# Kernel optimization log

Hardware: AMD Instinct MI355X
Metric: run time of the kernel (lower is better)

Reference implementation:

```python
import jax, jax.numpy as jnp
import numpy as np

N_NODES = 50000
N_EDGES = 800000
N_GRAPHS = 1024
NODE_IN = 128
HID = 300
DEPTH = 5
READOUT = 1024


def setup_inputs() -> dict:
    key = jax.random.key(0)
    ks = jax.random.split(key, 12)
    x = jax.random.normal(ks[0], (N_NODES, NODE_IN), dtype=jnp.float32)
    edge_index = jax.random.randint(ks[1], (2, N_EDGES), 0, N_NODES, dtype=jnp.int32)
    batch = jnp.sort(jax.random.randint(ks[2], (N_NODES,), 0, N_GRAPHS, dtype=jnp.int32))
    s_in = 1.0 / np.sqrt(NODE_IN)
    s_h = 1.0 / np.sqrt(HID)
    W_proj = jax.random.normal(ks[3], (NODE_IN, HID), dtype=jnp.float32) * s_in
    b_proj = jnp.zeros((HID,), dtype=jnp.float32)
    W1 = jax.random.normal(ks[4], (DEPTH, HID, HID), dtype=jnp.float32) * s_h
    b1 = jnp.zeros((DEPTH, HID), dtype=jnp.float32)
    W2 = jax.random.normal(ks[5], (DEPTH, HID, HID), dtype=jnp.float32) * s_h
    b2 = jnp.zeros((DEPTH, HID), dtype=jnp.float32)
    W_sp = jax.random.normal(ks[6], (HID, READOUT), dtype=jnp.float32) * s_h
    b_sp = jnp.zeros((READOUT,), dtype=jnp.float32)
    prelu_a = jnp.full((1,), 0.25, dtype=jnp.float32)  # nn.PReLU default
    return {"x": x, "edge_index": edge_index, "batch": batch,
            "W_proj": W_proj, "b_proj": b_proj, "W1": W1, "b1": b1,
            "W2": W2, "b2": b2, "W_sp": W_sp, "b_sp": b_sp, "prelu_a": prelu_a}


def reference(x, edge_index, batch, W_proj, b_proj, W1, b1, W2, b2, W_sp, b_sp, prelu_a):
    # project_node_feats: Linear + ReLU
    h = jax.nn.relu(x @ W_proj + b_proj)  # [N, HID]
    src = edge_index[0]
    dst = edge_index[1]
    for i in range(DEPTH):
        # GINConv (eps=0): out = nn(x + sum_{j in N(i)} x_j)
        agg = h + jax.ops.segment_sum(h[src], dst, num_segments=N_NODES)
        h = jax.nn.relu(agg @ W1[i] + b1[i]) @ W2[i] + b2[i]
        if i < DEPTH - 1:
            h = jax.nn.relu(h)
        # dropout is identity in eval mode
    # global_add_pool over graph ids
    pooled = jax.ops.segment_sum(h, batch, num_segments=N_GRAPHS)  # [G, HID]
    z = pooled @ W_sp + b_sp  # [G, READOUT]
    # PReLU with single shared parameter
    readout = jnp.where(z >= 0, z, prelu_a[0] * z)
    return readout
```

## Files before the change

kernel.cpp:

```cpp
#include <hip/hip_runtime.h>
#include <cstdint>

#define N_NODES 50000
#define N_EDGES 800000
#define N_GRAPHS 1024
#define NODE_IN 128
#define HID 300
#define DEPTH 5
#define READOUT 1024
#define PSTR 320

typedef float f32x4 __attribute__((ext_vector_type(4)));
typedef short bf16x8 __attribute__((ext_vector_type(8)));
typedef unsigned short us8 __attribute__((ext_vector_type(8)));

__device__ inline unsigned short f2bf(float v) {
    unsigned u = __float_as_uint(v);
    unsigned r = u + 0x7FFFu + ((u >> 16) & 1u);
    return (unsigned short)(r >> 16);
}
__device__ inline float bf2f(unsigned short h) {
    return __uint_as_float((unsigned)h << 16);
}
__device__ inline float bflo(unsigned u) { return __uint_as_float(u << 16); }
__device__ inline float bfhi(unsigned u) { return __uint_as_float(u & 0xFFFF0000u); }
__device__ inline unsigned packbf(float a, float b) {
    return (unsigned)f2bf(a) | ((unsigned)f2bf(b) << 16);
}

__global__ void hist2(const int* __restrict__ dst, int* __restrict__ cnt,
                      const int* __restrict__ batch, int* __restrict__ gcnt) {
    int i = blockIdx.x * blockDim.x + threadIdx.x;
    if (i < N_EDGES) atomicAdd(&cnt[dst[i]], 1);
    else if (i < N_EDGES + N_NODES) atomicAdd(&gcnt[batch[i - N_EDGES]], 1);
}

__global__ __launch_bounds__(256)
void scan_block2(const int* __restrict__ cnt, int* __restrict__ offs, int* __restrict__ bsum,
                 const int* __restrict__ gcnt, int* __restrict__ goffs, int* __restrict__ gsum,
                 int nbn) {
    __shared__ int buf[256];
    int b = blockIdx.x;
    const int* in; int* out; int* bs; int n; int bi;
    if (b < nbn) { in = cnt; out = offs; bs = bsum; n = N_NODES; bi = b; }
    else { in = gcnt; out = goffs; bs = gsum; n = N_GRAPHS; bi = b - nbn; }
    int i = bi * 256 + (int)threadIdx.x;
    int v = (i < n) ? in[i] : 0;
    buf[threadIdx.x] = v;
    __syncthreads();
    for (int off = 1; off < 256; off <<= 1) {
        int t = ((int)threadIdx.x >= off) ? buf[threadIdx.x - off] : 0;
        __syncthreads();
        buf[threadIdx.x] += t;
        __syncthreads();
    }
    if (i < n) out[i] = buf[threadIdx.x] - v;
    if (threadIdx.x == 255) bs[bi] = buf[255];
}

__global__ __launch_bounds__(256)
void scan_base2(const int* __restrict__ bsum, int* __restrict__ bbase, int nbn, int* __restrict__ tot_n,
                const int* __restrict__ gsum, int* __restrict__ gbase, int nbg, int* __restrict__ tot_g) {
    __shared__ int buf[256];
    const int* bs; int* bb; int nb; int* tot;
    if (blockIdx.x == 0) { bs = bsum; bb = bbase; nb = nbn; tot = tot_n; }
    else { bs = gsum; bb = gbase; nb = nbg; tot = tot_g; }
    int v = ((int)threadIdx.x < nb) ? bs[threadIdx.x] : 0;
    buf[threadIdx.x] = v;
    __syncthreads();
    for (int off = 1; off < 256; off <<= 1) {
        int t = ((int)threadIdx.x >= off) ? buf[threadIdx.x - off] : 0;
        __syncthreads();
        buf[threadIdx.x] += t;
        __syncthreads();
    }
    if ((int)threadIdx.x < nb) bb[threadIdx.x] = buf[threadIdx.x] - v;
    if (threadIdx.x == 255) *tot = buf[255];
}

__global__ void scan_add2(int* __restrict__ offs, const int* __restrict__ bbase,
                          int* __restrict__ cursor,
                          int* __restrict__ goffs, const int* __restrict__ gbase, int nbn) {
    int b = blockIdx.x;
    if (b < nbn) {
        int i = b * 256 + (int)threadIdx.x;
        if (i < N_NODES) {
            int o = offs[i] + bbase[b];
            offs[i] = o;
            cursor[i] = o;
        }
    } else {
        int bi = b - nbn;
        int i = bi * 256 + (int)threadIdx.x;
        if (i < N_GRAPHS) goffs[i] += gbase[bi];
    }
}

__global__ void scatter_kernel(const int* __restrict__ src, const int* __restrict__ dst,
                               int* __restrict__ cursor, int* __restrict__ csr, int n) {
    int i = blockIdx.x * blockDim.x + threadIdx.x;
    if (i < n) {
        int p = atomicAdd(&cursor[dst[i]], 1);
        csr[p] = src[i];
    }
}

__global__ __launch_bounds__(256)
void aggregate_bf16(const unsigned short* __restrict__ h, const int* __restrict__ offs,
                    const int* __restrict__ csr, unsigned short* __restrict__ out) {
    int wave = (int)((blockIdx.x * blockDim.x + threadIdx.x) >> 6);
    int lane = threadIdx.x & 63;
    if (wave >= N_NODES) return;
    float a0, a1, a2, a3, a4, a5;
    {
        const unsigned* r = (const unsigned*)(h + (size_t)wave * PSTR);
        uint2 u = *(const uint2*)&r[2 * lane];
        unsigned t = (lane < 32) ? r[128 + lane] : 0u;
        a0 = bflo(u.x); a1 = bfhi(u.x);
        a2 = bflo(u.y); a3 = bfhi(u.y);
        a4 = bflo(t);   a5 = bfhi(t);
    }
    int s = offs[wave], e = offs[wave + 1];
    int k = s;
    for (; k + 3 < e; k += 4) {
        const unsigned* r0 = (const unsigned*)(h + (size_t)csr[k] * PSTR);
        const unsigned* r1 = (const unsigned*)(h + (size_t)csr[k + 1] * PSTR);
        const unsigned* r2 = (const unsigned*)(h + (size_t)csr[k + 2] * PSTR);
        const unsigned* r3 = (const unsigned*)(h + (size_t)csr[k + 3] * PSTR);
        uint2 x0 = *(const uint2*)&r0[2 * lane];
        uint2 x1 = *(const uint2*)&r1[2 * lane];
        uint2 x2 = *(const uint2*)&r2[2 * lane];
        uint2 x3 = *(const uint2*)&r3[2 * lane];
        unsigned t0 = 0, t1 = 0, t2 = 0, t3 = 0;
        if (lane < 32) {
            t0 = r0[128 + lane]; t1 = r1[128 + lane];
            t2 = r2[128 + lane]; t3 = r3[128 + lane];
        }
        a0 += bflo(x0.x) + bflo(x1.x) + bflo(x2.x) + bflo(x3.x);
        a1 += bfhi(x0.x) + bfhi(x1.x) + bfhi(x2.x) + bfhi(x3.x);
        a2 += bflo(x0.y) + bflo(x1.y) + bflo(x2.y) + bflo(x3.y);
        a3 += bfhi(x0.y) + bfhi(x1.y) + bfhi(x2.y) + bfhi(x3.y);
        a4 += bflo(t0) + bflo(t1) + bflo(t2) + bflo(t3);
        a5 += bfhi(t0) + bfhi(t1) + bfhi(t2) + bfhi(t3);
    }
    for (; k < e; ++k) {
        const unsigned* r = (const unsigned*)(h + (size_t)csr[k] * PSTR);
        uint2 u = *(const uint2*)&r[2 * lane];
        unsigned t = (lane < 32) ? r[128 + lane] : 0u;
        a0 += bflo(u.x); a1 += bfhi(u.x);
        a2 += bflo(u.y); a3 += bfhi(u.y);
        a4 += bflo(t);   a5 += bfhi(t);
    }
    unsigned* o = (unsigned*)(out + (size_t)wave * PSTR);
    uint2 w; w.x = packbf(a0, a1); w.y = packbf(a2, a3);
    *(uint2*)&o[2 * lane] = w;
    if (lane < 32) o[128 + lane] = (lane < 22) ? packbf(a4, a5) : 0u;
}

__global__ __launch_bounds__(256)
void split_all(const float* __restrict__ W1, const float* __restrict__ W2,
               const float* __restrict__ Wsp, const float* __restrict__ Wproj,
               unsigned short* __restrict__ w1S, unsigned short* __restrict__ w2S,
               unsigned short* __restrict__ spH, unsigned short* __restrict__ spL,
               unsigned short* __restrict__ pjH, unsigned short* __restrict__ pjL) {
    __shared__ float tile[32][33];
    const int STK_SZ = 320 * 640;
    int z = blockIdx.z;
    const float* W;
    int K, N;
    if (z < 10) {
        if (blockIdx.x >= 10) return;
        int l = z % 5;
        W = (z < 5 ? W1 : W2) + (size_t)l * HID * HID;
        K = HID; N = HID;
    } else if (z == 10) {
        W = Wsp; K = HID; N = READOUT;
    } else {
        if (blockIdx.x >= 10 || blockIdx.y >= 4) return;
        W = Wproj; K = NODE_IN; N = HID;
    }
    int n0 = blockIdx.x * 32, k0 = blockIdx.y * 32;
    int tx = threadIdx.x & 31, ty = threadIdx.x >> 5;
#pragma unroll
    for (int r = 0; r < 4; ++r) {
        int k = k0 + ty + r * 8, n = n0 + tx;
        tile[ty + r * 8][tx] = (k < K && n < N) ? W[(size_t)k * N + n] : 0.f;
    }
    __syncthreads();
#pragma unroll
    for (int r = 0; r < 4; ++r) {
        int n = n0 + ty + r * 8, k = k0 + tx;
        float v = tile[tx][ty + r * 8];
        unsigned short hb = f2bf(v);
        unsigned short lb = f2bf(v - bf2f(hb));
        if (z < 10) {
            unsigned short* S = (z < 5 ? w1S : w2S) + (size_t)(z % 5) * STK_SZ;
            S[(size_t)n * 640 + k] = hb;
            S[(size_t)n * 640 + 320 + k] = lb;
        } else if (z == 10) {
            spH[(size_t)n * 320 + k] = hb;
            spL[(size_t)n * 320 + k] = lb;
        } else {
            pjH[(size_t)n * 128 + k] = hb;
            pjL[(size_t)n * 128 + k] = lb;
        }
    }
}

#define BSWZ(r, c) ((c) ^ (((r) >> 1) & 3))

__global__ __launch_bounds__(512, 1)
void gin_mlp_bk64(const unsigned short* __restrict__ Ap, int M,
                  const unsigned short* __restrict__ B1, const float* __restrict__ b1,
                  const unsigned short* __restrict__ B2, const float* __restrict__ b2,
                  unsigned short* __restrict__ Op, int act2) {
    __shared__ __align__(16) unsigned short At[128 * 320];
    __shared__ __align__(16) unsigned short Bs[2 * 320 * 64];

    const int tid = threadIdx.x;
    const int bm = blockIdx.x * 128;
    const int wid = tid >> 6, lane = tid & 63;
    const int wm = wid >> 2, wn = wid & 3;
    const int lr = lane & 15, lk = lane >> 4;

    float b1v[5], b2v[5];
#pragma unroll
    for (int n = 0; n < 5; ++n) {
        int col = wn * 80 + n * 16 + lr;
        b1v[n] = (col < HID) ? b1[col] : 0.f;
        b2v[n] = (col < HID) ? b2[col] : 0.f;
    }

    size_t bofs[10]; int bldso[10];
#pragma unroll
    for (int i = 0; i < 10; ++i) {
        int q = i * 512 + tid;
        int half = q >= 2560;
        int q2 = q - half * 2560;
        int r = q2 >> 3, c = q2 & 7;
        bofs[i] = (size_t)r * 640 + half * 320 + c * 8;
        bldso[i] = half * 20480 + r * 64 + ((c ^ (r & 7)) * 8);
    }

    us8 vB[10];
    auto LOADB = [&](const unsigned short* B, int t) {
        int k0 = t * 64;
#pragma unroll
        for (int i = 0; i < 10; ++i)
            vB[i] = *(const us8*)&B[bofs[i] + k0];
    };

    LOADB(B1, 0);

#pragma unroll
    for (int i = 0; i < 10; ++i) {
        int g = i * 512 + tid;
        int row = g / 40, c = g - row * 40;
        int grow = bm + row; if (grow >= M) grow = M - 1;
        us8 v = *(const us8*)&Ap[(size_t)grow * PSTR + c * 8];
        *(us8*)&At[row * 320 + (c ^ (row & 7)) * 8] = v;
    }

    f32x4 acc[4][5];

    auto RUN = [&](const unsigned short* B) {
        for (int t = 0; t < 5; ++t) {
            __syncthreads();
#pragma unroll
            for (int i = 0; i < 10; ++i) *(us8*)&Bs[bldso[i]] = vB[i];
            if (t < 4) LOADB(B, t + 1);
            __syncthreads();
#pragma unroll
            for (int kk = 0; kk < 2; ++kk) {
                bf16x8 aS[4];
                int ac = t * 8 + kk * 4 + lk;
#pragma unroll
                for (int m = 0; m < 4; ++m) {
                    int row = wm * 64 + m * 16 + lr;
                    aS[m] = *(const bf16x8*)&At[row * 320 + (ac ^ (row & 7)) * 8];
                }
                int bc = kk * 4 + lk;
#pragma unroll
                for (int n = 0; n < 5; ++n) {
                    int rb = wn * 80 + n * 16 + lr;
                    int so = rb * 64 + ((bc ^ (rb & 7)) * 8);
                    bf16x8 bh = *(const bf16x8*)&Bs[so];
                    bf16x8 bl = *(const bf16x8*)&Bs[20480 + so];
#pragma unroll
                    for (int m = 0; m < 4; ++m) {
                        acc[m][n] = __builtin_amdgcn_mfma_f32_16x16x32_bf16(aS[m], bh, acc[m][n], 0, 0, 0);
                        acc[m][n] = __builtin_amdgcn_mfma_f32_16x16x32_bf16(aS[m], bl, acc[m][n], 0, 0, 0);
                    }
                }
            }
        }
    };

#pragma unroll
    for (int m = 0; m < 4; ++m)
#pragma unroll
        for (int n = 0; n < 5; ++n) acc[m][n] = (f32x4)0.f;
    RUN(B1);

    LOADB(B2, 0);

    __syncthreads();
#pragma unroll
    for (int n = 0; n < 5; ++n) {
        int col = wn * 80 + n * 16 + lr;
        int cc = col >> 3, cp = col & 7;
        float bv = b1v[n];
        bool vc = col < HID;
#pragma unroll
        for (int m = 0; m < 4; ++m) {
#pragma unroll
            for (int p = 0; p < 4; ++p) {
                int row = wm * 64 + m * 16 + lk * 4 + p;
                float v = vc ? fmaxf(acc[m][n][p] + bv, 0.f) : 0.f;
                At[row * 320 + ((cc ^ (row & 7)) * 8) + cp] = f2bf(v);
            }
        }
    }

#pragma unroll
    for (int m = 0; m < 4; ++m)
#pragma unroll
        for (int n = 0; n < 5; ++n) acc[m][n] = (f32x4)0.f;
    RUN(B2);

    __syncthreads();
#pragma unroll
    for (int n = 0; n < 5; ++n) {
        int col = wn * 80 + n * 16 + lr;
        int cc = col >> 3, cp = col & 7;
        float bv = b2v[n];
        bool vc = col < HID;
#pragma unroll
        for (int m = 0; m < 4; ++m) {
#pragma unroll
            for (int p = 0; p < 4; ++p) {
                int row = wm * 64 + m * 16 + lk * 4 + p;
                float v = vc ? (acc[m][n][p] + bv) : 0.f;
                if (act2) v = fmaxf(v, 0.f);
                At[row * 320 + ((cc ^ (row & 7)) * 8) + cp] = f2bf(v);
            }
        }
    }
    __syncthreads();
#pragma unroll
    for (int i = 0; i < 10; ++i) {
        int g = i * 512 + tid;
        int row = g / 40, c = g - row * 40;
        int grow = bm + row;
        if (grow < M)
            *(us8*)&Op[(size_t)grow * PSTR + c * 8] =
                *(const us8*)&At[row * 320 + (c ^ (row & 7)) * 8];
    }
}

__global__ __launch_bounds__(256)
void gemm_f32A(const float* __restrict__ A, int lda, int M, int K, int KP,
               const unsigned short* __restrict__ BH, const unsigned short* __restrict__ BL, int KPB,
               const float* __restrict__ bias, int N,
               float* __restrict__ C, int ldc, unsigned short* __restrict__ Op, int outPlane,
               int act, const float* __restrict__ prelu) {
    __shared__ __align__(16) unsigned short AsH[64 * 40];
    __shared__ __align__(16) unsigned short AsL[64 * 40];
    __shared__ __align__(16) unsigned short BsH[320 * 40];
    __shared__ __align__(16) unsigned short BsL[320 * 40];

    const int tid = threadIdx.x;
    const int bm = blockIdx.y * 64;
    const int bn = blockIdx.x * 320;
    const int wid = tid >> 6, lane = tid & 63;
    const int lr = lane & 15, lk = lane >> 4;
    const int ar = tid >> 2, ac = tid & 3;

    f32x4 acc[4][5];
#pragma unroll
    for (int m = 0; m < 4; ++m)
#pragma unroll
        for (int n = 0; n < 5; ++n) acc[m][n] = (f32x4)0.f;

    for (int k0 = 0; k0 < KP; k0 += 32) {
        {
            int gm = bm + ar;
            int k = k0 + ac * 8;
            float v[8];
#pragma unroll
            for (int j = 0; j < 8; ++j) v[j] = 0.f;
            if (gm < M) {
                if (k + 7 < K) {
                    float4 p0 = *(const float4*)&A[(size_t)gm * lda + k];
                    float4 p1 = *(const float4*)&A[(size_t)gm * lda + k + 4];
                    v[0] = p0.x; v[1] = p0.y; v[2] = p0.z; v[3] = p0.w;
                    v[4] = p1.x; v[5] = p1.y; v[6] = p1.z; v[7] = p1.w;
                } else {
#pragma unroll
                    for (int j = 0; j < 8; ++j)
                        if (k + j < K) v[j] = A[(size_t)gm * lda + k + j];
                }
            }
            us8 h, l;
#pragma unroll
            for (int j = 0; j < 8; ++j) {
                unsigned short hb = f2bf(v[j]);
                h[j] = hb;
                l[j] = f2bf(v[j] - bf2f(hb));
            }
            *(us8*)&AsH[ar * 40 + ac * 8] = h;
            *(us8*)&AsL[ar * 40 + ac * 8] = l;
        }
#pragma unroll
        for (int p = 0; p < 5; ++p) {
            int r = ar + p * 64;
            size_t gb = (size_t)(bn + r) * KPB + k0 + ac * 8;
            *(us8*)&BsH[r * 40 + ac * 8] = *(const us8*)&BH[gb];
            *(us8*)&BsL[r * 40 + ac * 8] = *(const us8*)&BL[gb];
        }
        __syncthreads();
        bf16x8 aH[4], aL[4];
#pragma unroll
        for (int m = 0; m < 4; ++m) {
            aH[m] = *(const bf16x8*)&AsH[(m * 16 + lr) * 40 + lk * 8];
            aL[m] = *(const bf16x8*)&AsL[(m * 16 + lr) * 40 + lk * 8];
        }
#pragma unroll
        for (int n = 0; n < 5; ++n) {
            int r = wid * 80 + n * 16 + lr;
            bf16x8 bh = *(const bf16x8*)&BsH[r * 40 + lk * 8];
            bf16x8 bl = *(const bf16x8*)&BsL[r * 40 + lk * 8];
#pragma unroll
            for (int m = 0; m < 4; ++m) {
                acc[m][n] = __builtin_amdgcn_mfma_f32_16x16x32_bf16(aH[m], bh, acc[m][n], 0, 0, 0);
                acc[m][n] = __builtin_amdgcn_mfma_f32_16x16x32_bf16(aH[m], bl, acc[m][n], 0, 0, 0);
                acc[m][n] = __builtin_amdgcn_mfma_f32_16x16x32_bf16(aL[m], bh, acc[m][n], 0, 0, 0);
            }
        }
        __syncthreads();
    }
    float slope = (act == 2) ? prelu[0] : 0.f;
#pragma unroll
    for (int n = 0; n < 5; ++n) {
        int col = bn + wid * 80 + n * 16 + lr;
        bool vc = col < N;
        float bv = vc ? bias[col] : 0.f;
#pragma unroll
        for (int m = 0; m < 4; ++m) {
            int rbase = bm + m * 16 + lk * 4;
#pragma unroll
            for (int p = 0; p < 4; ++p) {
                int row = rbase + p;
                if (row >= M) continue;
                float v = vc ? (acc[m][n][p] + bv) : 0.f;
                if (act == 1) v = fmaxf(v, 0.f);
                else if (act == 2) v = (v >= 0.f) ? v : slope * v;
                if (outPlane) {
                    if (col < PSTR) Op[(size_t)row * PSTR + col] = f2bf(v);
                } else if (vc) {
                    C[(size_t)row * ldc + col] = v;
                }
            }
        }
    }
}

__global__ __launch_bounds__(128)
void pool_seg(const unsigned short* __restrict__ h, const int* __restrict__ goffs,
              float* __restrict__ pooled) {
    __shared__ float red[6 * 64];
    int g = blockIdx.x;
    int w = threadIdx.x >> 6, lane = threadIdx.x & 63;
    int s = goffs[g], e = goffs[g + 1];
    float a0 = 0.f, a1 = 0.f, a2 = 0.f, a3 = 0.f, a4 = 0.f, a5 = 0.f;
    for (int node = s + w; node < e; node += 2) {
        const unsigned* r = (const unsigned*)(h + (size_t)node * PSTR);
        uint2 u = *(const uint2*)&r[2 * lane];
        unsigned t = (lane < 32) ? r[128 + lane] : 0u;
        a0 += bflo(u.x); a1 += bfhi(u.x);
        a2 += bflo(u.y); a3 += bfhi(u.y);
        a4 += bflo(t);   a5 += bfhi(t);
    }
    if (w == 1) {
        red[lane] = a0;        red[64 + lane] = a1;
        red[128 + lane] = a2;  red[192 + lane] = a3;
        red[256 + lane] = a4;  red[320 + lane] = a5;
    }
    __syncthreads();
    if (w == 0) {
        a0 += red[lane];        a1 += red[64 + lane];
        a2 += red[128 + lane];  a3 += red[192 + lane];
        a4 += red[256 + lane];  a5 += red[320 + lane];
        float* pr = pooled + (size_t)g * PSTR;
        *(float4*)&pr[4 * lane] = make_float4(a0, a1, a2, a3);
        if (lane < 32) *(float2*)&pr[256 + 2 * lane] = make_float2(a4, a5);
    }
}

extern "C" void kernel_launch(void* const* d_in, const int* in_sizes, int n_in,
                              void* d_out, int out_size, void* d_ws, size_t ws_size,
                              hipStream_t stream) {
    const float* x      = (const float*)d_in[0];
    const int*   eidx   = (const int*)d_in[1];
    const int*   batch  = (const int*)d_in[2];
    const float* W_proj = (const float*)d_in[3];
    const float* b_proj = (const float*)d_in[4];
    const float* W1     = (const float*)d_in[5];
    const float* b1     = (const float*)d_in[6];
    const float* W2     = (const float*)d_in[7];
    const float* b2     = (const float*)d_in[8];
    const float* W_sp   = (const float*)d_in[9];
    const float* b_sp   = (const float*)d_in[10];
    const float* prelu  = (const float*)d_in[11];

    const int* src = eidx;
    const int* dst = eidx + N_EDGES;

    const size_t PLANE = (size_t)N_NODES * PSTR + 64;
    const int STK_SZ = 320 * 640;
    const int SP_SZ  = 1280 * 320;
    const int PJ_SZ  = 320 * 128;
    const int NB  = (N_NODES + 255) / 256;
    const int NBG = (N_GRAPHS + 255) / 256;

    unsigned short* hA  = (unsigned short*)d_ws;
    unsigned short* hB  = hA + PLANE;
    float* pooled = (float*)(hB + PLANE);
    unsigned short* w1S = (unsigned short*)(pooled + (size_t)N_GRAPHS * PSTR + 16);
    unsigned short* w2S = w1S + 5 * (size_t)STK_SZ;
    unsigned short* spH = w2S + 5 * (size_t)STK_SZ;
    unsigned short* spL = spH + SP_SZ;
    unsigned short* pjH = spL + SP_SZ;
    unsigned short* pjL = pjH + PJ_SZ;
    int* cnt    = (int*)(((uintptr_t)(pjL + PJ_SZ) + 15) & ~(uintptr_t)15);
    int* gcnt   = cnt + N_NODES;
    int* bsum   = gcnt + N_GRAPHS;
    int* bbase  = bsum + 256;
    int* gsum   = bbase + 256;
    int* gbase  = gsum + 256;
    int* offs   = gbase + 256;
    int* goffs  = offs + N_NODES + 1;
    int* cursor = goffs + N_GRAPHS + 1;
    int* csr    = cursor + N_NODES;
    size_t needed = (size_t)((uintptr_t)(csr + N_EDGES) - (uintptr_t)d_ws);
    if (ws_size < needed) return;

    split_all<<<dim3(40, 10, 12), 256, 0, stream>>>(W1, W2, W_sp, W_proj,
                                                    w1S, w2S, spH, spL, pjH, pjL);

    hipMemsetAsync(cnt, 0, (N_NODES + N_GRAPHS) * sizeof(int), stream);
    hist2<<<(N_EDGES + N_NODES + 255) / 256, 256, 0, stream>>>(dst, cnt, batch, gcnt);
    scan_block2<<<NB + NBG, 256, 0, stream>>>(cnt, offs, bsum, gcnt, goffs, gsum, NB);
    scan_base2<<<2, 256, 0, stream>>>(bsum, bbase, NB, offs + N_NODES,
                                      gsum, gbase, NBG, goffs + N_GRAPHS);
    scan_add2<<<NB + NBG, 256, 0, stream>>>(offs, bbase, cursor, goffs, gbase, NB);
    scatter_kernel<<<(N_EDGES + 255) / 256, 256, 0, stream>>>(src, dst, cursor, csr, N_EDGES);

    gemm_f32A<<<dim3(1, (N_NODES + 63) / 64), 256, 0, stream>>>(
        x, NODE_IN, N_NODES, NODE_IN, 128, pjH, pjL, 128,
        b_proj, HID, nullptr, 0, hA, 1, 1, nullptr);

    const int GBM = (N_NODES + 127) / 128;
    unsigned short* cur = hA;
    unsigned short* agp = hB;
    for (int i = 0; i < DEPTH; ++i) {
        aggregate_bf16<<<(N_NODES * 64 + 255) / 256, 256, 0, stream>>>(cur, offs, csr, agp);
        gin_mlp_bk64<<<GBM, 512, 0, stream>>>(
            agp, N_NODES,
            w1S + (size_t)i * STK_SZ, b1 + (size_t)i * HID,
            w2S + (size_t)i * STK_SZ, b2 + (size_t)i * HID,
            cur, (i < DEPTH - 1) ? 1 : 0);
    }

    pool_seg<<<N_GRAPHS, 128, 0, stream>>>(cur, goffs, pooled);

    gemm_f32A<<<dim3(4, (N_GRAPHS + 63) / 64), 256, 0, stream>>>(
        pooled, PSTR, N_GRAPHS, HID, 320, spH, spL, 320,
        b_sp, READOUT, (float*)d_out, READOUT, nullptr, 0, 2, prelu);
}
```

Baseline: 1.033 ms.

## Use 16-byte gathers in aggregation and shrink MLP K-tile to raise occupancy

The aggregation kernel now has 40 lanes per wave each load 16 bytes per neighbour row, replacing the split 8-byte plus 4-byte loads, so each gathered row needs fewer memory instructions. The fused MLP kernel moves from a K-tile of 64 to 32 with separate hi/lo weight planes. This halves the shared-memory B buffer and drops the one-block-per-CU launch bound, so more blocks can be resident on each CU. The cost is twice as many barrier-separated K iterations and 24 idle lanes per wave in aggregation.

Result: faster. 945.2 us (-8.5%).

```diff
diff --git a/kernel.cpp b/kernel.cpp
--- a/kernel.cpp
+++ b/kernel.cpp
@@ -111,73 +111,73 @@
     int wave = (int)((blockIdx.x * blockDim.x + threadIdx.x) >> 6);
     int lane = threadIdx.x & 63;
     if (wave >= N_NODES) return;
-    float a0, a1, a2, a3, a4, a5;
-    {
-        const unsigned* r = (const unsigned*)(h + (size_t)wave * PSTR);
-        uint2 u = *(const uint2*)&r[2 * lane];
-        unsigned t = (lane < 32) ? r[128 + lane] : 0u;
-        a0 = bflo(u.x); a1 = bfhi(u.x);
-        a2 = bflo(u.y); a3 = bfhi(u.y);
-        a4 = bflo(t);   a5 = bfhi(t);
+    bool act = lane < 40;
+    size_t lo = (size_t)lane * 8;
+    float a0 = 0.f, a1 = 0.f, a2 = 0.f, a3 = 0.f, a4 = 0.f, a5 = 0.f, a6 = 0.f, a7 = 0.f;
+    if (act) {
+        uint4 v = *(const uint4*)(h + (size_t)wave * PSTR + lo);
+        a0 = bflo(v.x); a1 = bfhi(v.x); a2 = bflo(v.y); a3 = bfhi(v.y);
+        a4 = bflo(v.z); a5 = bfhi(v.z); a6 = bflo(v.w); a7 = bfhi(v.w);
     }
     int s = offs[wave], e = offs[wave + 1];
     int k = s;
     for (; k + 3 < e; k += 4) {
-        const unsigned* r0 = (const unsigned*)(h + (size_t)csr[k] * PSTR);
-        const unsigned* r1 = (const unsigned*)(h + (size_t)csr[k + 1] * PSTR);
-        const unsigned* r2 = (const unsigned*)(h + (size_t)csr[k + 2] * PSTR);
-        const unsigned* r3 = (const unsigned*)(h + (size_t)csr[k + 3] * PSTR);
-        uint2 x0 = *(const uint2*)&r0[2 * lane];
-        uint2 x1 = *(const uint2*)&r1[2 * lane];
-        uint2 x2 = *(const uint2*)&r2[2 * lane];
-        uint2 x3 = *(const uint2*)&r3[2 * lane];
-        unsigned t0 = 0, t1 = 0, t2 = 0, t3 = 0;
-        if (lane < 32) {
-            t0 = r0[128 + lane]; t1 = r1[128 + lane];
-            t2 = r2[128 + lane]; t3 = r3[128 + lane];
-        }
-        a0 += bflo(x0.x) + bflo(x1.x) + bflo(x2.x) + bflo(x3.x);
-        a1 += bfhi(x0.x) + bfhi(x1.x) + bfhi(x2.x) + bfhi(x3.x);
-        a2 += bflo(x0.y) + bflo(x1.y) + bflo(x2.y) + bflo(x3.y);
-        a3 += bfhi(x0.y) + bfhi(x1.y) + bfhi(x2.y) + bfhi(x3.y);
-        a4 += bflo(t0) + bflo(t1) + bflo(t2) + bflo(t3);
-        a5 += bfhi(t0) + bfhi(t1) + bfhi(t2) + bfhi(t3);
+        int i0 = csr[k], i1 = csr[k + 1], i2 = csr[k + 2], i3 = csr[k + 3];
+        if (act) {
+            uint4 v0 = *(const uint4*)(h + (size_t)i0 * PSTR + lo);
+            uint4 v1 = *(const uint4*)(h + (size_t)i1 * PSTR + lo);
+            uint4 v2 = *(const uint4*)(h + (size_t)i2 * PSTR + lo);
+            uint4 v3 = *(const uint4*)(h + (size_t)i3 * PSTR + lo);
+            a0 += bflo(v0.x) + bflo(v1.x) + bflo(v2.x) + bflo(v3.x);
+            a1 += bfhi(v0.x) + bfhi(v1.x) + bfhi(v2.x) + bfhi(v3.x);
+            a2 += bflo(v0.y) + bflo(v1.y) + bflo(v2.y) + bflo(v3.y);
+            a3 += bfhi(v0.y) + bfhi(v1.y) + bfhi(v2.y) + bfhi(v3.y);
+            a4 += bflo(v0.z) + bflo(v1.z) + bflo(v2.z) + bflo(v3.z);
+            a5 += bfhi(v0.z) + bfhi(v1.z) + bfhi(v2.z) + bfhi(v3.z);
+            a6 += bflo(v0.w) + bflo(v1.w) + bflo(v2.w) + bflo(v3.w);
+            a7 += bfhi(v0.w) + bfhi(v1.w) + bfhi(v2.w) + bfhi(v3.w);
+        }
     }
     for (; k < e; ++k) {
-        const unsigned* r = (const unsigned*)(h + (size_t)csr[k] * PSTR);
-        uint2 u = *(const uint2*)&r[2 * lane];
-        unsigned t = (lane < 32) ? r[128 + lane] : 0u;
-        a0 += bflo(u.x); a1 += bfhi(u.x);
-        a2 += bflo(u.y); a3 += bfhi(u.y);
-        a4 += bflo(t);   a5 += bfhi(t);
-    }
-    unsigned* o = (unsigned*)(out + (size_t)wave * PSTR);
-    uint2 w; w.x = packbf(a0, a1); w.y = packbf(a2, a3);
-    *(uint2*)&o[2 * lane] = w;
-    if (lane < 32) o[128 + lane] = (lane < 22) ? packbf(a4, a5) : 0u;
+        int i0 = csr[k];
+        if (act) {
+            uint4 v = *(const uint4*)(h + (size_t)i0 * PSTR + lo);
+            a0 += bflo(v.x); a1 += bfhi(v.x); a2 += bflo(v.y); a3 += bfhi(v.y);
+            a4 += bflo(v.z); a5 += bfhi(v.z); a6 += bflo(v.w); a7 += bfhi(v.w);
+        }
+    }
+    if (act) {
+        uint4 w;
+        w.x = packbf(a0, a1); w.y = packbf(a2, a3);
+        w.z = packbf(a4, a5); w.w = packbf(a6, a7);
+        *(uint4*)(out + (size_t)wave * PSTR + lo) = w;
+    }
 }
 
 __global__ __launch_bounds__(256)
 void split_all(const float* __restrict__ W1, const float* __restrict__ W2,
                const float* __restrict__ Wsp, const float* __restrict__ Wproj,
-               unsigned short* __restrict__ w1S, unsigned short* __restrict__ w2S,
+               unsigned short* __restrict__ w1H, unsigned short* __restrict__ w1L,
+               unsigned short* __restrict__ w2H, unsigned short* __restrict__ w2L,
                unsigned short* __restrict__ spH, unsigned short* __restrict__ spL,
                unsigned short* __restrict__ pjH, unsigned short* __restrict__ pjL) {
     __shared__ float tile[32][33];
-    const int STK_SZ = 320 * 640;
+    const int LAYER_SZ = 320 * 320;
     int z = blockIdx.z;
-    const float* W;
-    int K, N;
+    const float* W; unsigned short* H; unsigned short* L;
+    int K, N, KP;
     if (z < 10) {
         if (blockIdx.x >= 10) return;
         int l = z % 5;
         W = (z < 5 ? W1 : W2) + (size_t)l * HID * HID;
-        K = HID; N = HID;
+        H = (z < 5 ? w1H : w2H) + (size_t)l * LAYER_SZ;
+        L = (z < 5 ? w1L : w2L) + (size_t)l * LAYER_SZ;
+        K = HID; N = HID; KP = 320;
     } else if (z == 10) {
-        W = Wsp; K = HID; N = READOUT;
+        W = Wsp; H = spH; L = spL; K = HID; N = READOUT; KP = 320;
     } else {
         if (blockIdx.x >= 10 || blockIdx.y >= 4) return;
-        W = Wproj; K = NODE_IN; N = HID;
+        W = Wproj; H = pjH; L = pjL; K = NODE_IN; N = HID; KP = 128;
     }
     int n0 = blockIdx.x * 32, k0 = blockIdx.y * 32;
     int tx = threadIdx.x & 31, ty = threadIdx.x >> 5;
@@ -192,30 +192,22 @@
         int n = n0 + ty + r * 8, k = k0 + tx;
         float v = tile[tx][ty + r * 8];
         unsigned short hb = f2bf(v);
-        unsigned short lb = f2bf(v - bf2f(hb));
-        if (z < 10) {
-            unsigned short* S = (z < 5 ? w1S : w2S) + (size_t)(z % 5) * STK_SZ;
-            S[(size_t)n * 640 + k] = hb;
-            S[(size_t)n * 640 + 320 + k] = lb;
-        } else if (z == 10) {
-            spH[(size_t)n * 320 + k] = hb;
-            spL[(size_t)n * 320 + k] = lb;
-        } else {
-            pjH[(size_t)n * 128 + k] = hb;
-            pjL[(size_t)n * 128 + k] = lb;
-        }
+        H[(size_t)n * KP + k] = hb;
+        L[(size_t)n * KP + k] = f2bf(v - bf2f(hb));
     }
 }
 
 #define BSWZ(r, c) ((c) ^ (((r) >> 1) & 3))
 
-__global__ __launch_bounds__(512, 1)
-void gin_mlp_bk64(const unsigned short* __restrict__ Ap, int M,
-                  const unsigned short* __restrict__ B1, const float* __restrict__ b1,
-                  const unsigned short* __restrict__ B2, const float* __restrict__ b2,
-                  unsigned short* __restrict__ Op, int act2) {
+__global__ __launch_bounds__(512)
+void gin_mlp(const unsigned short* __restrict__ Ap, int M,
+             const unsigned short* __restrict__ B1H, const unsigned short* __restrict__ B1L,
+             const float* __restrict__ b1,
+             const unsigned short* __restrict__ B2H, const unsigned short* __restrict__ B2L,
+             const float* __restrict__ b2,
+             unsigned short* __restrict__ Op, int act2) {
     __shared__ __align__(16) unsigned short At[128 * 320];
-    __shared__ __align__(16) unsigned short Bs[2 * 320 * 64];
+    __shared__ __align__(16) unsigned short Bs[2 * 10240];
 
     const int tid = threadIdx.x;
     const int bm = blockIdx.x * 128;
@@ -231,26 +223,29 @@
         b2v[n] = (col < HID) ? b2[col] : 0.f;
     }
 
-    size_t bofs[10]; int bldso[10];
-#pragma unroll
-    for (int i = 0; i < 10; ++i) {
-        int q = i * 512 + tid;
-        int half = q >= 2560;
-        int q2 = q - half * 2560;
-        int r = q2 >> 3, c = q2 & 7;
-        bofs[i] = (size_t)r * 640 + half * 320 + c * 8;
-        bldso[i] = half * 20480 + r * 64 + ((c ^ (r & 7)) * 8);
-    }
-
-    us8 vB[10];
-    auto LOADB = [&](const unsigned short* B, int t) {
-        int k0 = t * 64;
-#pragma unroll
-        for (int i = 0; i < 10; ++i)
-            vB[i] = *(const us8*)&B[bofs[i] + k0];
+    size_t bofs[5]; int bldso[5]; bool bpl[5];
+#pragma unroll
+    for (int i = 0; i < 5; ++i) {
+        int qq = i * 512 + tid;
+        bool pl = qq >= 1280;
+        int q2 = qq - (pl ? 1280 : 0);
+        int r = q2 >> 2, c = q2 & 3;
+        bpl[i] = pl;
+        bofs[i] = (size_t)r * 320 + c * 8;
+        bldso[i] = (pl ? 10240 : 0) + r * 32 + BSWZ(r, c) * 8;
+    }
+
+    us8 vB[5];
+    auto LOADB = [&](const unsigned short* BH, const unsigned short* BL, int t) {
+        int k0 = t * 32;
+#pragma unroll
+        for (int i = 0; i < 5; ++i) {
+            const unsigned short* base = bpl[i] ? BL : BH;
+            vB[i] = *(const us8*)&base[bofs[i] + k0];
+        }
     };
 
-    LOADB(B1, 0);
+    LOADB(B1H, B1L, 0);
 
 #pragma unroll
     for (int i = 0; i < 10; ++i) {
@@ -263,35 +258,31 @@
 
     f32x4 acc[4][5];
 
-    auto RUN = [&](const unsigned short* B) {
-        for (int t = 0; t < 5; ++t) {
+    auto RUN = [&](const unsigned short* BH, const unsigned short* BL) {
+        for (int t = 0; t < 10; ++t) {
             __syncthreads();
 #pragma unroll
-            for (int i = 0; i < 10; ++i) *(us8*)&Bs[bldso[i]] = vB[i];
-            if (t < 4) LOADB(B, t + 1);
+            for (int i = 0; i < 5; ++i) *(us8*)&Bs[bldso[i]] = vB[i];
+            if (t < 9) LOADB(BH, BL, t + 1);
             __syncthreads();
-#pragma unroll
-            for (int kk = 0; kk < 2; ++kk) {
-                bf16x8 aS[4];
-                int ac = t * 8 + kk * 4 + lk;
+            bf16x8 aS[4];
+#pragma unroll
+            for (int m = 0; m < 4; ++m) {
+                int row = wm * 64 + m * 16 + lr;
+                int c = t * 4 + lk;
+                aS[m] = *(const bf16x8*)&At[row * 320 + (c ^ (row & 7)) * 8];
+            }
+#pragma unroll
+            for (int n = 0; n < 5; ++n) {
+                int rb = wn * 80 + n * 16 + lr;
+                int sc = rb * 32 + BSWZ(rb, lk) * 8;
+                bf16x8 bh = *(const bf16x8*)&Bs[sc];
+                bf16x8 bl = *(const bf16x8*)&Bs[10240 + sc];
 #pragma unroll
                 for (int m = 0; m < 4; ++m) {
-                    int row = wm * 64 + m * 16 + lr;
-                    aS[m] = *(const bf16x8*)&At[row * 320 + (ac ^ (row & 7)) * 8];
+                    acc[m][n] = __builtin_amdgcn_mfma_f32_16x16x32_bf16(aS[m], bh, acc[m][n], 0, 0, 0);
+                    acc[m][n] = __builtin_amdgcn_mfma_f32_16x16x32_bf16(aS[m], bl, acc[m][n], 0, 0, 0);
                 }
-                int bc = kk * 4 + lk;
-#pragma unroll
-                for (int n = 0; n < 5; ++n) {
-                    int rb = wn * 80 + n * 16 + lr;
-                    int so = rb * 64 + ((bc ^ (rb & 7)) * 8);
-                    bf16x8 bh = *(const bf16x8*)&Bs[so];
-                    bf16x8 bl = *(const bf16x8*)&Bs[20480 + so];
-#pragma unroll
-                    for (int m = 0; m < 4; ++m) {
-                        acc[m][n] = __builtin_amdgcn_mfma_f32_16x16x32_bf16(aS[m], bh, acc[m][n], 0, 0, 0);
-                        acc[m][n] = __builtin_amdgcn_mfma_f32_16x16x32_bf16(aS[m], bl, acc[m][n], 0, 0, 0);
-                    }
-                }
             }
         }
     };
@@ -300,9 +291,9 @@
     for (int m = 0; m < 4; ++m)
 #pragma unroll
         for (int n = 0; n < 5; ++n) acc[m][n] = (f32x4)0.f;
-    RUN(B1);
-
-    LOADB(B2, 0);
+    RUN(B1H, B1L);
+
+    LOADB(B2H, B2L, 0);
 
     __syncthreads();
 #pragma unroll
@@ -326,7 +317,7 @@
     for (int m = 0; m < 4; ++m)
 #pragma unroll
         for (int n = 0; n < 5; ++n) acc[m][n] = (f32x4)0.f;
-    RUN(B2);
+    RUN(B2H, B2L);
 
     __syncthreads();
 #pragma unroll
@@ -517,7 +508,7 @@
     const int* dst = eidx + N_EDGES;
 
     const size_t PLANE = (size_t)N_NODES * PSTR + 64;
-    const int STK_SZ = 320 * 640;
+    const int LAYER_SZ = 320 * 320;
     const int SP_SZ  = 1280 * 320;
     const int PJ_SZ  = 320 * 128;
     const int NB  = (N_NODES + 255) / 256;
@@ -526,9 +517,11 @@
     unsigned short* hA  = (unsigned short*)d_ws;
     unsigned short* hB  = hA + PLANE;
     float* pooled = (float*)(hB + PLANE);
-    unsigned short* w1S = (unsigned short*)(pooled + (size_t)N_GRAPHS * PSTR + 16);
-    unsigned short* w2S = w1S + 5 * (size_t)STK_SZ;
-    unsigned short* spH = w2S + 5 * (size_t)STK_SZ;
+    unsigned short* w1H = (unsigned short*)(pooled + (size_t)N_GRAPHS * PSTR + 16);
+    unsigned short* w1L = w1H + 5 * (size_t)LAYER_SZ;
+    unsigned short* w2H = w1L + 5 * (size_t)LAYER_SZ;
+    unsigned short* w2L = w2H + 5 * (size_t)LAYER_SZ;
+    unsigned short* spH = w2L + 5 * (size_t)LAYER_SZ;
     unsigned short* spL = spH + SP_SZ;
     unsigned short* pjH = spL + SP_SZ;
     unsigned short* pjL = pjH + PJ_SZ;
@@ -546,7 +539,7 @@
     if (ws_size < needed) return;
 
     split_all<<<dim3(40, 10, 12), 256, 0, stream>>>(W1, W2, W_sp, W_proj,
-                                                    w1S, w2S, spH, spL, pjH, pjL);
+                                                    w1H, w1L, w2H, w2L, spH, spL, pjH, pjL);
 
     hipMemsetAsync(cnt, 0, (N_NODES + N_GRAPHS) * sizeof(int), stream);
     hist2<<<(N_EDGES + N_NODES + 255) / 256, 256, 0, stream>>>(dst, cnt, batch, gcnt);
@@ -565,10 +558,10 @@
     unsigned short* agp = hB;
     for (int i = 0; i < DEPTH; ++i) {
         aggregate_bf16<<<(N_NODES * 64 + 255) / 256, 256, 0, stream>>>(cur, offs, csr, agp);
-        gin_mlp_bk64<<<GBM, 512, 0, stream>>>(
+        gin_mlp<<<GBM, 512, 0, stream>>>(
             agp, N_NODES,
-            w1S + (size_t)i * STK_SZ, b1 + (size_t)i * HID,
-            w2S + (size_t)i * STK_SZ, b2 + (size_t)i * HID,
+            w1H + (size_t)i * LAYER_SZ, w1L + (size_t)i * LAYER_SZ, b1 + (size_t)i * HID,
+            w2H + (size_t)i * LAYER_SZ, w2L + (size_t)i * LAYER_SZ, b2 + (size_t)i * HID,
             cur, (i < DEPTH - 1) ? 1 : 0);
     }
 
```
